# Kernel optimization log

Measured on AMD Instinct MI355X. Metric: run time of the kernel, lower is better.

The kernel has to match this reference:

```python
import jax, jax.numpy as jnp
import numpy as np

B, A, NC, DIR, LMAX, MAXZ, NORB = 8, 64, 128, 4, 2, 10, 14
NF = NC * DIR * (2 * LMAX + 1)   # 2560
O2 = NORB * NORB                 # 196
AO = A * NORB                    # 896
LOG2 = float(np.log(2.0))

def ssp(v):  # spk shifted softplus
    return jax.nn.softplus(v) - LOG2

def setup_inputs():
    key = jax.random.key(0)
    ks = jax.random.split(key, 12)
    Z = jax.random.randint(ks[0], (B, A), 1, MAXZ)
    idx = np.arange(A)
    nbh_np = np.stack([np.delete(idx, i) for i in range(A)], 0)  # [A, A-1]: all atoms except self
    nbh = jnp.asarray(np.broadcast_to(nbh_np[None], (B, A, A - 1)).copy(), dtype=jnp.int32)
    x = jax.random.normal(ks[1], (B, A, NC), jnp.float32)
    Vijkl = jax.random.normal(ks[2], (B, A, A - 1, NF), jnp.float32) * 0.1
    sc = 1.0 / np.sqrt(NF)
    W_off = jax.random.normal(ks[3], (NF, O2), jnp.float32) * sc
    b_off = jnp.zeros((O2,), jnp.float32)
    W_on = jax.random.normal(ks[4], (NF, O2), jnp.float32) * sc
    b_on = jnp.zeros((O2,), jnp.float32)
    W_ovoff = jax.random.normal(ks[5], (NF, O2), jnp.float32) * sc
    b_ovoff = jnp.zeros((O2,), jnp.float32)
    ov_emb = jax.random.normal(ks[6], (MAXZ, O2), jnp.float32) * 0.1  # trainable overlap onsite embedding
    orb_energies = jax.random.normal(ks[7], (MAXZ, NORB), jnp.float32)  # h0 energies
    s0_energies = jnp.ones((MAXZ, NORB), jnp.float32)                   # s0 init = ones
    W1 = jax.random.normal(ks[8], (NC, NC // 2), jnp.float32) / np.sqrt(NC)
    b1 = jnp.zeros((NC // 2,), jnp.float32)
    W2 = jax.random.normal(ks[9], (NC // 2, 1), jnp.float32) / np.sqrt(NC // 2)
    b2 = jnp.zeros((1,), jnp.float32)
    return {"Z": Z, "nbh": nbh, "x": x, "Vijkl": Vijkl,
            "W_off": W_off, "b_off": b_off, "W_on": W_on, "b_on": b_on,
            "W_ovoff": W_ovoff, "b_ovoff": b_ovoff, "ov_emb": ov_emb,
            "orb_energies": orb_energies, "s0_energies": s0_energies,
            "W1": W1, "b1": b1, "W2": W2, "b2": b2}

def reference(Z, nbh, x, Vijkl, W_off, b_off, W_on, b_on, W_ovoff, b_ovoff,
              ov_emb, orb_energies, s0_energies, W1, b1, W2, b2):
    # permutation that reorders neighbor slots (plus appended zero/self slot) into atom order
    ar = jnp.broadcast_to(jnp.arange(A, dtype=nbh.dtype)[None, :, None], (B, A, 1))
    sort_idx = jnp.argsort(jnp.concatenate([nbh, ar], axis=2), axis=2)  # [B,A,A]
    eyeA = jnp.eye(A, dtype=Vijkl.dtype)
    eyeAO = jnp.eye(AO, dtype=Vijkl.dtype)

    def assemble(off, on):
        # off: [B,A,A-1,O2] pair blocks; on: [B,A,O2] onsite blocks
        offz = jnp.concatenate([off, jnp.zeros((B, A, 1, O2), off.dtype)], axis=2)  # zero self block at slot A-1
        offg = jnp.take_along_axis(offz, sort_idx[..., None], axis=2)               # [B,A,A,O2]
        M = offg + eyeA[None, :, :, None] * on[:, :, None, :]
        M = M.reshape(B, A, A, NORB, NORB).transpose(0, 1, 3, 2, 4).reshape(B, AO, AO)
        return 0.5 * (M + M.transpose(0, 2, 1))

    # Hamiltonian: offsite Dense + onsite Dense mean-aggregated over pairs
    H_off = Vijkl @ W_off + b_off                       # [B,A,A-1,O2]
    H_on = jnp.mean(Vijkl @ W_on + b_on, axis=2)        # [B,A,O2]
    H = assemble(H_off, H_on)
    # h0 single-atom diagonal (orb mask is all-active -> full diagonal)
    H = H + eyeAO[None] * orb_energies[Z].reshape(B, 1, AO)

    # Overlap: offsite Dense + onsite embedding lookup
    S_off = Vijkl @ W_ovoff + b_ovoff
    S_on = ov_emb[Z]                                    # [B,A,O2]
    S = assemble(S_off, S_on)
    S = S + eyeAO[None] * s0_energies[Z].reshape(B, 1, AO)

    # energy head: Dense->ssp->Dense->ScaleShift(0,1), sum over atoms
    Ei = ssp(x @ W1 + b1) @ W2 + b2                     # [B,A,1]
    E = jnp.sum(Ei, axis=1)                             # [B,1]
    return H, S, E
```

## Files before the change

kernel.cpp:

```cpp
#include <hip/hip_runtime.h>

#define B_      8
#define A_      64
#define NPAIR   63
#define NC_     128
#define NF_     2560
#define O2_     196
#define NORB_   14
#define AO_     896
#define NCOLS   588
#define NSTORE  392
#define CSTRIDE 400
#define KSTEPS  80
#define NMACRO  20
#define BM      126
#define BN      640
#define MAC_BYTES 81920

typedef float f32x4 __attribute__((ext_vector_type(4)));
typedef int   v8i   __attribute__((ext_vector_type(8)));
typedef int   v4i   __attribute__((ext_vector_type(4)));

#define SCA 0x7F7F7F7F
#define SCB 0x7C7C7C7C

__device__ __forceinline__ unsigned f2bf(float f) {
    unsigned u = __builtin_bit_cast(unsigned, f);
    return (u + 0x7fffu + ((u >> 16) & 1u)) >> 16;
}

__global__ __launch_bounds__(512)
void prep_energy(const float* __restrict__ W_off, const float* __restrict__ W_ovoff,
                 const float* __restrict__ W_on, unsigned char* __restrict__ Bws,
                 const float* __restrict__ x, const float* __restrict__ W1,
                 const float* __restrict__ b1, const float* __restrict__ W2,
                 const float* __restrict__ b2, float* __restrict__ E) {
    const int t = threadIdx.x;
    if (blockIdx.x < KSTEPS) {
        __shared__ float wt[32 * BN];
        const int ks = blockIdx.x;
        for (int e = t; e < 32 * BN; e += 512) {
            int kl = e / BN, c = e - kl * BN;
            int kg = ks * 32 + kl;
            float v = 0.f;
            if (c < O2_)          v = W_off  [(size_t)kg * O2_ + c];
            else if (c < 2 * O2_) v = W_ovoff[(size_t)kg * O2_ + (c - O2_)];
            else if (c < 3 * O2_) v = W_on   [(size_t)kg * O2_ + (c - 2 * O2_)];
            wt[kl * BN + c] = v * 8.0f;
        }
        __syncthreads();
        unsigned char* out = Bws + (size_t)(ks >> 2) * MAC_BYTES + (ks & 3) * 32;
        for (int u = t; u < BN * 8; u += 512) {
            int n = u >> 3, q = u & 7;
            int w = __builtin_amdgcn_cvt_pk_fp8_f32(wt[(q*4+0)*BN+n], wt[(q*4+1)*BN+n], 0, false);
            w     = __builtin_amdgcn_cvt_pk_fp8_f32(wt[(q*4+2)*BN+n], wt[(q*4+3)*BN+n], w, true);
            *(int*)(out + (size_t)n * 128 + q * 4) = w;
        }
    } else {
        __shared__ float partial[8];
        const int b = blockIdx.x - KSTEPS;
        const int lane = t & 63;
        const int w = t >> 6;
        float esum = 0.f;
        for (int aa = 0; aa < 8; ++aa) {
            const int a = w * 8 + aa;
            const float* xr = x + (size_t)(b * A_ + a) * NC_;
            float hj = b1[lane];
            for (int k = 0; k < NC_; ++k) hj = fmaf(xr[k], W1[k * 64 + lane], hj);
            float sp = fmaxf(hj, 0.f) + log1pf(expf(-fabsf(hj))) - 0.69314718055994531f;
            float v = sp * W2[lane];
            for (int off = 32; off; off >>= 1) v += __shfl_down(v, off);
            if (lane == 0) esum += v + b2[0];
        }
        if (lane == 0) partial[w] = esum;
        __syncthreads();
        if (t == 0) {
            float e = 0.f;
            for (int k = 0; k < 8; ++k) e += partial[k];
            E[b] = e;
        }
    }
}

__global__ __launch_bounds__(512, 2)
void gemm_off(const float* __restrict__ V, const unsigned char* __restrict__ Bws,
              const float* __restrict__ b_off, const float* __restrict__ b_ovoff,
              const float* __restrict__ b_on, float* __restrict__ HSoff,
              float* __restrict__ Hon) {
    __shared__ alignas(16) float Af32[8][4096];
    __shared__ alignas(16) unsigned char Afp8[4 * 6144];
    __shared__ float HonLds[2][O2_];

    const int tid  = threadIdx.x;
    const int mt   = blockIdx.x;
    const int lane = tid & 63;
    const int wv   = tid >> 6;
    const int wm   = wv >> 2, wn = wv & 3;
    const int wvu  = __builtin_amdgcn_readfirstlane(wv);

    const int r0  = tid >> 3;
    const int r1c = (64 + r0) > 125 ? 125 : (64 + r0);
    const int sg  = tid & 7;
    const float* asrc0 = V + (size_t)(mt * BM + r0)  * NF_ + sg * 4;
    const float* asrc1 = V + (size_t)(mt * BM + r1c) * NF_ + sg * 4;

    const unsigned char* bbase = Bws + ((size_t)(wn * 160 + (lane & 15))) * 128 + (lane >> 4) * 32;
#define BLD(T_, nf_) (*(const v8i*)(bbase + (size_t)(T_) * MAC_BYTES + (nf_) * 2048))

    const unsigned aoff = (unsigned)(lane >> 4) * 6144 + (unsigned)(wm * 64 + (lane & 15)) * 48;

    f32x4 acc[4][10];
#pragma unroll
    for (int mf = 0; mf < 4; ++mf)
#pragma unroll
        for (int nf = 0; nf < 10; ++nf)
            acc[mf][nf] = (f32x4){0.f, 0.f, 0.f, 0.f};

    auto stage = [&](int slot, int k32) {
        __builtin_amdgcn_global_load_lds(
            (const __attribute__((address_space(1))) void*)(asrc0 + (size_t)k32 * 32),
            (__attribute__((address_space(3))) void*)(&Af32[slot][wvu * 256]), 16, 0, 0);
        __builtin_amdgcn_global_load_lds(
            (const __attribute__((address_space(1))) void*)(asrc1 + (size_t)k32 * 32),
            (__attribute__((address_space(3))) void*)(&Af32[slot][2048 + wvu * 256]), 16, 0, 0);
    };
    auto conv = [&](int slot, int sub) {
        const char* sp = (const char*)&Af32[slot][0];
        float4 f0 = *(const float4*)(sp + tid * 16);
        float4 f1 = *(const float4*)(sp + tid * 16 + 8192);
        int w0 = __builtin_amdgcn_cvt_pk_fp8_f32(f0.x, f0.y, 0, false);
        w0     = __builtin_amdgcn_cvt_pk_fp8_f32(f0.z, f0.w, w0, true);
        int w1 = __builtin_amdgcn_cvt_pk_fp8_f32(f1.x, f1.y, 0, false);
        w1     = __builtin_amdgcn_cvt_pk_fp8_f32(f1.z, f1.w, w1, true);
        *(int*)&Afp8[sub * 6144 + (tid >> 3) * 48 + (tid & 7) * 4] = w0;
        *(int*)&Afp8[sub * 6144 + (64 + (tid >> 3)) * 48 + (tid & 7) * 4] = w1;
    };

    union AV { v4i h[2]; v8i v; };
#define AFLD(dst_, mf_) { AV a_; \
    a_.h[0] = *(const v4i*)&Afp8[aoff + (mf_) * 768];      \
    a_.h[1] = *(const v4i*)&Afp8[aoff + (mf_) * 768 + 16]; \
    dst_ = a_.v; }

#define MFMA1(abf_, bq_, mf_, nf_) \
    acc[mf_][nf_] = __builtin_amdgcn_mfma_scale_f32_16x16x128_f8f6f4( \
        abf_, bq_, acc[mf_][nf_], 0, 0, 0, SCA, 0, SCB);

#define C4(bv_, nf_) { \
    __builtin_amdgcn_s_setprio(1); \
    MFMA1(af0, bv_, 0, nf_); MFMA1(af1, bv_, 1, nf_); \
    MFMA1(af2, bv_, 2, nf_); MFMA1(af3, bv_, 3, nf_); \
    __builtin_amdgcn_s_setprio(0); }

    v8i b0, b1, b2, b3, b4, af0, af1, af2, af3;

    stage(0, 0); stage(1, 1); stage(2, 2); stage(3, 3);
    b0 = BLD(0, 0); b1 = BLD(0, 1); b2 = BLD(0, 2); b3 = BLD(0, 3); b4 = BLD(0, 4);

    for (int T = 0; T < NMACRO; ++T) {
        const int sb = (T & 1) * 4;
        const int st = ((T + 1) & 1) * 4;
#pragma unroll
        for (int i = 0; i < 4; ++i) {
            asm volatile("s_waitcnt vmcnt(16)" ::: "memory");
            __builtin_amdgcn_sched_barrier(0);
            if (T < NMACRO - 1) stage(st + i, 4 * (T + 1) + i);
            else                stage(st + i, 76 + i);
            conv(sb + i, i);
        }
        asm volatile("s_waitcnt lgkmcnt(0)" ::: "memory");
        __builtin_amdgcn_sched_barrier(0);
        __builtin_amdgcn_s_barrier();
        __builtin_amdgcn_sched_barrier(0);

        AFLD(af0, 0); AFLD(af1, 1); AFLD(af2, 2); AFLD(af3, 3);
        C4(b0, 0); b0 = BLD(T, 5);
        C4(b1, 1); b1 = BLD(T, 6);
        C4(b2, 2); b2 = BLD(T, 7);
        C4(b3, 3); b3 = BLD(T, 8);
        C4(b4, 4); b4 = BLD(T, 9);
        C4(b0, 5); b0 = BLD(T + 1, 0);
        C4(b1, 6); b1 = BLD(T + 1, 1);
        C4(b2, 7); b2 = BLD(T + 1, 2);
        C4(b3, 8); b3 = BLD(T + 1, 3);
        C4(b4, 9); b4 = BLD(T + 1, 4);
        __builtin_amdgcn_sched_barrier(0);
        __builtin_amdgcn_s_barrier();
        __builtin_amdgcn_sched_barrier(0);
    }

    if (tid < 2 * O2_) HonLds[tid / O2_][tid % O2_] = 0.f;
    __syncthreads();

    const int c16 = lane & 15, rg = lane >> 4;
#pragma unroll
    for (int nf = 0; nf < 10; ++nf) {
        const int C = wn * 160 + nf * 16 + c16;
        if (C >= NSTORE) continue;
        const float bias = (C < O2_) ? b_off[C] : b_ovoff[C - O2_];
#pragma unroll
        for (int mf = 0; mf < 4; ++mf) {
            const int L = wm * 64 + mf * 16 + rg * 4;
#pragma unroll
            for (int jj = 0; jj < 4; ++jj) {
                const int row = L + jj;
                if (row < BM)
                    HSoff[(size_t)(mt * BM + row) * CSTRIDE + C] = acc[mf][nf][jj] + bias;
            }
        }
    }
#pragma unroll
    for (int nf = 0; nf < 10; ++nf) {
        const int C = wn * 160 + nf * 16 + c16;
        if (C < NSTORE || C >= NCOLS) continue;
        const int cc = C - NSTORE;
        float s0 = 0.f, s1 = 0.f;
#pragma unroll
        for (int mf = 0; mf < 4; ++mf) {
            const int L = wm * 64 + mf * 16 + rg * 4;
#pragma unroll
            for (int jj = 0; jj < 4; ++jj) {
                const int row = L + jj;
                const float v = acc[mf][nf][jj];
                if (row < NPAIR)       s0 += v;
                else if (row < BM)     s1 += v;
            }
        }
        s0 += __shfl_down(s0, 32); s0 += __shfl_down(s0, 16);
        s1 += __shfl_down(s1, 32); s1 += __shfl_down(s1, 16);
        if (lane < 16) {
            atomicAdd(&HonLds[0][cc], s0);
            atomicAdd(&HonLds[1][cc], s1);
        }
    }
    __syncthreads();
    if (tid < 2 * O2_) {
        const int atom = tid / O2_, c = tid % O2_;
        Hon[(size_t)(mt * 2 + atom) * O2_ + c] =
            HonLds[atom][c] * (1.f / (float)NPAIR) + b_on[c];
    }
#undef BLD
#undef AFLD
#undef MFMA1
#undef C4
}

__global__ __launch_bounds__(256)
void assemble_k(const float* __restrict__ HSoff, const float* __restrict__ Hon,
                const int* __restrict__ Z, const float* __restrict__ ov_emb,
                const float* __restrict__ orbE, const float* __restrict__ s0E,
                float* __restrict__ H, float* __restrict__ S) {
    __shared__ float Ai[NPAIR * 197];
    __shared__ float Bj[2][16 * 200];
    __shared__ float Dg[O2_];
    __shared__ float Dd[NORB_];

    const int bid = blockIdx.x;
    const int h = bid & 1, i = (bid >> 1) & 63, b = bid >> 7;
    const int t = threadIdx.x;
    const int g = b * A_ + i;
    const int z = Z[g];
    float* out = (h ? S : H) + (size_t)b * AO_ * AO_;

    const float* abase = HSoff + (size_t)g * NPAIR * CSTRIDE + h * O2_;
    for (int u = t; u < NPAIR * O2_; u += 256) {
        int jj = u / O2_, e = u - jj * O2_;
        Ai[jj * 197 + e] = abase[(size_t)jj * CSTRIDE + e];
    }
    if (t < O2_)   Dg[t] = h ? ov_emb[(size_t)z * O2_ + t]   : Hon[(size_t)g * O2_ + t];
    if (t < NORB_) Dd[t] = h ? s0E[(size_t)z * NORB_ + t]    : orbE[(size_t)z * NORB_ + t];

    auto stageB = [&](int buf, int jc) {
        for (int u = t; u < 16 * O2_; u += 256) {
            int jl = u / O2_, e = u - jl * O2_;
            int j = jc * 16 + jl;
            if (j != i) {
                int idx = (i < j) ? i : i - 1;
                Bj[buf][jl * 200 + e] =
                    HSoff[((size_t)(b * A_ + j) * NPAIR + idx) * CSTRIDE + h * O2_ + e];
            }
        }
    };
    stageB(0, 0);
    __syncthreads();

    const int tj = t / NORB_, tq = t - tj * NORB_;
    for (int jc = 0; jc < 4; ++jc) {
        if (jc < 3) stageB((jc + 1) & 1, jc + 1);
        if (t < 224) {
            const int j = jc * 16 + tj;
            const int cur = jc & 1;
#pragma unroll
            for (int p = 0; p < NORB_; ++p) {
                float v;
                if (j == i) {
                    v = 0.5f * (Dg[p * NORB_ + tq] + Dg[tq * NORB_ + p]);
                    if (p == tq) v += Dd[p];
                } else {
                    int jj = (j < i) ? j : j - 1;
                    v = 0.5f * (Ai[jj * 197 + p * NORB_ + tq] + Bj[cur][tj * 200 + tq * NORB_ + p]);
                }
                out[(size_t)(i * NORB_ + p) * AO_ + jc * 224 + t] = v;
            }
        }
        __syncthreads();
    }
}

extern "C" void kernel_launch(void* const* d_in, const int* in_sizes, int n_in,
                              void* d_out, int out_size, void* d_ws, size_t ws_size,
                              hipStream_t stream) {
    const int*   Z       = (const int*)  d_in[0];
    const float* x       = (const float*)d_in[2];
    const float* V       = (const float*)d_in[3];
    const float* W_off   = (const float*)d_in[4];
    const float* b_off   = (const float*)d_in[5];
    const float* W_on    = (const float*)d_in[6];
    const float* b_on    = (const float*)d_in[7];
    const float* W_ovoff = (const float*)d_in[8];
    const float* b_ovoff = (const float*)d_in[9];
    const float* ov_emb  = (const float*)d_in[10];
    const float* orbE    = (const float*)d_in[11];
    const float* s0E     = (const float*)d_in[12];
    const float* W1      = (const float*)d_in[13];
    const float* b1      = (const float*)d_in[14];
    const float* W2      = (const float*)d_in[15];
    const float* b2      = (const float*)d_in[16];

    float* H = (float*)d_out;
    float* S = H + (size_t)B_ * AO_ * AO_;
    float* E = S + (size_t)B_ * AO_ * AO_;

    char* ws = (char*)d_ws;
    unsigned char* Bws = (unsigned char*)ws;
    float* HSoff = (float*)(ws + (size_t)4  * 1024 * 1024);
    float* Hon   = (float*)(ws + (size_t)60 * 1024 * 1024);

    prep_energy<<<KSTEPS + B_, 512, 0, stream>>>(W_off, W_ovoff, W_on, Bws,
                                                 x, W1, b1, W2, b2, E);
    gemm_off   <<<256,  512, 0, stream>>>(V, Bws, b_off, b_ovoff, b_on, HSoff, Hon);
    assemble_k <<<1024, 256, 0, stream>>>(HSoff, Hon, Z, ov_emb, orbE, s0E, H, S);
}
```

Before: 288.2 us.

## Pre-convert V to swizzled fp8 tiles in prep kernel, simplify GEMM pipeline

Moves the fp32-to-fp8 conversion of the activation matrix out of the GEMM main loop into a separate bandwidth-bound pass in the prep kernel. That pass writes fp8 tiles with an XOR-swizzled layout, and the GEMM loads them directly into LDS with double buffering and no per-step conversion. This removes the LDS round trip and conversion work from the MFMA loop. In exchange it adds an extra write and read of an ~80MB fp8 intermediate in global memory.

```diff
diff --git a/kernel.cpp b/kernel.cpp
--- a/kernel.cpp
+++ b/kernel.cpp
@@ -16,10 +16,10 @@
 #define BM      126
 #define BN      640
 #define MAC_BYTES 81920
+#define ATILE   16384
 
 typedef float f32x4 __attribute__((ext_vector_type(4)));
 typedef int   v8i   __attribute__((ext_vector_type(8)));
-typedef int   v4i   __attribute__((ext_vector_type(4)));
 
 #define SCA 0x7F7F7F7F
 #define SCB 0x7C7C7C7C
@@ -30,11 +30,12 @@
 }
 
 __global__ __launch_bounds__(512)
-void prep_energy(const float* __restrict__ W_off, const float* __restrict__ W_ovoff,
-                 const float* __restrict__ W_on, unsigned char* __restrict__ Bws,
-                 const float* __restrict__ x, const float* __restrict__ W1,
-                 const float* __restrict__ b1, const float* __restrict__ W2,
-                 const float* __restrict__ b2, float* __restrict__ E) {
+void prep_all(const float* __restrict__ W_off, const float* __restrict__ W_ovoff,
+              const float* __restrict__ W_on, unsigned char* __restrict__ Bws,
+              const float* __restrict__ x, const float* __restrict__ W1,
+              const float* __restrict__ b1, const float* __restrict__ W2,
+              const float* __restrict__ b2, float* __restrict__ E,
+              const float* __restrict__ V, unsigned char* __restrict__ Aws) {
     const int t = threadIdx.x;
     if (blockIdx.x < KSTEPS) {
         __shared__ float wt[32 * BN];
@@ -56,7 +57,7 @@
             w     = __builtin_amdgcn_cvt_pk_fp8_f32(wt[(q*4+2)*BN+n], wt[(q*4+3)*BN+n], w, true);
             *(int*)(out + (size_t)n * 128 + q * 4) = w;
         }
-    } else {
+    } else if (blockIdx.x < KSTEPS + B_) {
         __shared__ float partial[8];
         const int b = blockIdx.x - KSTEPS;
         const int lane = t & 63;
@@ -79,16 +80,35 @@
             for (int k = 0; k < 8; ++k) e += partial[k];
             E[b] = e;
         }
+    } else {
+        const int u = (blockIdx.x - KSTEPS - B_) * 512 + t;
+        const int R = u / 160, c16 = u - R * 160;
+        const float* src = V + (size_t)R * NF_ + c16 * 16;
+        float4 f0 = ((const float4*)src)[0];
+        float4 f1 = ((const float4*)src)[1];
+        float4 f2 = ((const float4*)src)[2];
+        float4 f3 = ((const float4*)src)[3];
+        int4 w;
+        w.x = __builtin_amdgcn_cvt_pk_fp8_f32(f0.x, f0.y, 0, false);
+        w.x = __builtin_amdgcn_cvt_pk_fp8_f32(f0.z, f0.w, w.x, true);
+        w.y = __builtin_amdgcn_cvt_pk_fp8_f32(f1.x, f1.y, 0, false);
+        w.y = __builtin_amdgcn_cvt_pk_fp8_f32(f1.z, f1.w, w.y, true);
+        w.z = __builtin_amdgcn_cvt_pk_fp8_f32(f2.x, f2.y, 0, false);
+        w.z = __builtin_amdgcn_cvt_pk_fp8_f32(f2.z, f2.w, w.z, true);
+        w.w = __builtin_amdgcn_cvt_pk_fp8_f32(f3.x, f3.y, 0, false);
+        w.w = __builtin_amdgcn_cvt_pk_fp8_f32(f3.z, f3.w, w.w, true);
+        const int mtile = R / BM, row = R - mtile * BM;
+        const int T = c16 >> 3, s = c16 & 7;
+        *(int4*)(Aws + ((size_t)(mtile * NMACRO + T) << 14) + row * 128 + s * 16) = w;
     }
 }
 
 __global__ __launch_bounds__(512, 2)
-void gemm_off(const float* __restrict__ V, const unsigned char* __restrict__ Bws,
+void gemm_off(const unsigned char* __restrict__ Aws, const unsigned char* __restrict__ Bws,
               const float* __restrict__ b_off, const float* __restrict__ b_ovoff,
               const float* __restrict__ b_on, float* __restrict__ HSoff,
               float* __restrict__ Hon) {
-    __shared__ alignas(16) float Af32[8][4096];
-    __shared__ alignas(16) unsigned char Afp8[4 * 6144];
+    __shared__ alignas(16) unsigned char Afp8[2][ATILE];
     __shared__ float HonLds[2][O2_];
 
     const int tid  = threadIdx.x;
@@ -98,16 +118,18 @@
     const int wm   = wv >> 2, wn = wv & 3;
     const int wvu  = __builtin_amdgcn_readfirstlane(wv);
 
-    const int r0  = tid >> 3;
-    const int r1c = (64 + r0) > 125 ? 125 : (64 + r0);
-    const int sg  = tid & 7;
-    const float* asrc0 = V + (size_t)(mt * BM + r0)  * NF_ + sg * 4;
-    const float* asrc1 = V + (size_t)(mt * BM + r1c) * NF_ + sg * 4;
+    const int row0 = tid >> 3, seg = tid & 7;
+    const int row1 = 64 + row0, rowc1 = row1 > 125 ? 125 : row1;
+    const unsigned off0 = (unsigned)(row0 * 128 + (((seg >> 1) ^ (row0 & 3)) << 5) + (seg & 1) * 16);
+    const unsigned off1 = (unsigned)(rowc1 * 128 + (((seg >> 1) ^ (rowc1 & 3)) << 5) + (seg & 1) * 16);
+    const unsigned char* atile0 = Aws + (size_t)mt * NMACRO * ATILE;
 
     const unsigned char* bbase = Bws + ((size_t)(wn * 160 + (lane & 15))) * 128 + (lane >> 4) * 32;
 #define BLD(T_, nf_) (*(const v8i*)(bbase + (size_t)(T_) * MAC_BYTES + (nf_) * 2048))
 
-    const unsigned aoff = (unsigned)(lane >> 4) * 6144 + (unsigned)(wm * 64 + (lane & 15)) * 48;
+    const unsigned abase = (unsigned)(wm * 64 * 128 + (lane & 15) * 128 +
+                                      (((lane >> 4) ^ (lane & 3)) << 5));
+#define AFLD(dst_, buf_, mf_) dst_ = *(const v8i*)&Afp8[buf_][abase + (mf_) * 2048];
 
     f32x4 acc[4][10];
 #pragma unroll
@@ -116,31 +138,15 @@
         for (int nf = 0; nf < 10; ++nf)
             acc[mf][nf] = (f32x4){0.f, 0.f, 0.f, 0.f};
 
-    auto stage = [&](int slot, int k32) {
+    auto stage = [&](int buf, int T) {
+        const unsigned char* tp = atile0 + (size_t)T * ATILE;
         __builtin_amdgcn_global_load_lds(
-            (const __attribute__((address_space(1))) void*)(asrc0 + (size_t)k32 * 32),
-            (__attribute__((address_space(3))) void*)(&Af32[slot][wvu * 256]), 16, 0, 0);
+            (const __attribute__((address_space(1))) void*)(tp + off0),
+            (__attribute__((address_space(3))) void*)(&Afp8[buf][wvu * 1024]), 16, 0, 0);
         __builtin_amdgcn_global_load_lds(
-            (const __attribute__((address_space(1))) void*)(asrc1 + (size_t)k32 * 32),
-            (__attribute__((address_space(3))) void*)(&Af32[slot][2048 + wvu * 256]), 16, 0, 0);
+            (const __attribute__((address_space(1))) void*)(tp + off1),
+            (__attribute__((address_space(3))) void*)(&Afp8[buf][8192 + wvu * 1024]), 16, 0, 0);
     };
-    auto conv = [&](int slot, int sub) {
-        const char* sp = (const char*)&Af32[slot][0];
-        float4 f0 = *(const float4*)(sp + tid * 16);
-        float4 f1 = *(const float4*)(sp + tid * 16 + 8192);
-        int w0 = __builtin_amdgcn_cvt_pk_fp8_f32(f0.x, f0.y, 0, false);
-        w0     = __builtin_amdgcn_cvt_pk_fp8_f32(f0.z, f0.w, w0, true);
-        int w1 = __builtin_amdgcn_cvt_pk_fp8_f32(f1.x, f1.y, 0, false);
-        w1     = __builtin_amdgcn_cvt_pk_fp8_f32(f1.z, f1.w, w1, true);
-        *(int*)&Afp8[sub * 6144 + (tid >> 3) * 48 + (tid & 7) * 4] = w0;
-        *(int*)&Afp8[sub * 6144 + (64 + (tid >> 3)) * 48 + (tid & 7) * 4] = w1;
-    };
-
-    union AV { v4i h[2]; v8i v; };
-#define AFLD(dst_, mf_) { AV a_; \
-    a_.h[0] = *(const v4i*)&Afp8[aoff + (mf_) * 768];      \
-    a_.h[1] = *(const v4i*)&Afp8[aoff + (mf_) * 768 + 16]; \
-    dst_ = a_.v; }
 
 #define MFMA1(abf_, bq_, mf_, nf_) \
     acc[mf_][nf_] = __builtin_amdgcn_mfma_scale_f32_16x16x128_f8f6f4( \
@@ -154,26 +160,21 @@
 
     v8i b0, b1, b2, b3, b4, af0, af1, af2, af3;
 
-    stage(0, 0); stage(1, 1); stage(2, 2); stage(3, 3);
+    stage(0, 0);
     b0 = BLD(0, 0); b1 = BLD(0, 1); b2 = BLD(0, 2); b3 = BLD(0, 3); b4 = BLD(0, 4);
-
+    asm volatile("s_waitcnt vmcnt(5)" ::: "memory");
+    __builtin_amdgcn_sched_barrier(0);
+    __builtin_amdgcn_s_barrier();
+    __builtin_amdgcn_sched_barrier(0);
+
+    int cur = 0;
     for (int T = 0; T < NMACRO; ++T) {
-        const int sb = (T & 1) * 4;
-        const int st = ((T + 1) & 1) * 4;
-#pragma unroll
-        for (int i = 0; i < 4; ++i) {
-            asm volatile("s_waitcnt vmcnt(16)" ::: "memory");
-            __builtin_amdgcn_sched_barrier(0);
-            if (T < NMACRO - 1) stage(st + i, 4 * (T + 1) + i);
-            else                stage(st + i, 76 + i);
-            conv(sb + i, i);
-        }
+        AFLD(af0, cur, 0); AFLD(af1, cur, 1); AFLD(af2, cur, 2); AFLD(af3, cur, 3);
         asm volatile("s_waitcnt lgkmcnt(0)" ::: "memory");
         __builtin_amdgcn_sched_barrier(0);
-        __builtin_amdgcn_s_barrier();
-        __builtin_amdgcn_sched_barrier(0);
-
-        AFLD(af0, 0); AFLD(af1, 1); AFLD(af2, 2); AFLD(af3, 3);
+
+        stage(cur ^ 1, T + 1 < NMACRO ? T + 1 : NMACRO - 1);
+
         C4(b0, 0); b0 = BLD(T, 5);
         C4(b1, 1); b1 = BLD(T, 6);
         C4(b2, 2); b2 = BLD(T, 7);
@@ -184,9 +185,12 @@
         C4(b2, 7); b2 = BLD(T + 1, 2);
         C4(b3, 8); b3 = BLD(T + 1, 3);
         C4(b4, 9); b4 = BLD(T + 1, 4);
+
+        asm volatile("s_waitcnt vmcnt(10)" ::: "memory");
         __builtin_amdgcn_sched_barrier(0);
         __builtin_amdgcn_s_barrier();
         __builtin_amdgcn_sched_barrier(0);
+        cur ^= 1;
     }
 
     if (tid < 2 * O2_) HonLds[tid / O2_][tid % O2_] = 0.f;
@@ -333,11 +337,13 @@
 
     char* ws = (char*)d_ws;
     unsigned char* Bws = (unsigned char*)ws;
-    float* HSoff = (float*)(ws + (size_t)4  * 1024 * 1024);
-    float* Hon   = (float*)(ws + (size_t)60 * 1024 * 1024);
-
-    prep_energy<<<KSTEPS + B_, 512, 0, stream>>>(W_off, W_ovoff, W_on, Bws,
-                                                 x, W1, b1, W2, b2, E);
-    gemm_off   <<<256,  512, 0, stream>>>(V, Bws, b_off, b_ovoff, b_on, HSoff, Hon);
-    assemble_k <<<1024, 256, 0, stream>>>(HSoff, Hon, Z, ov_emb, orbE, s0E, H, S);
-}
+    unsigned char* Aws = (unsigned char*)(ws + (size_t)4 * 1024 * 1024);
+    float* HSoff = (float*)(ws + (size_t)88  * 1024 * 1024);
+    float* Hon   = (float*)(ws + (size_t)142 * 1024 * 1024);
+
+    const int conv_blocks = (32256 * 160) / 512;
+    prep_all  <<<KSTEPS + B_ + conv_blocks, 512, 0, stream>>>(
+        W_off, W_ovoff, W_on, Bws, x, W1, b1, W2, b2, E, V, Aws);
+    gemm_off  <<<256,  512, 0, stream>>>(Aws, Bws, b_off, b_ovoff, b_on, HSoff, Hon);
+    assemble_k<<<1024, 256, 0, stream>>>(HSoff, Hon, Z, ov_emb, orbE, s0E, H, S);
+}
```

New measurement: 271.3 us. 5.8% less time.

## Restructure A-tile staging into fp32 ring plus swizzled double-buffered fp8 tile

Applied to the files above, without the earlier changes.

Replaces the 8-slot fp32 staging buffer and interleaved per-substep convert loop with a 4-slot fp32 ring and a double-buffered fp8 A tile. All four k-substeps of the next macro step are loaded at once, and the fp8 conversion runs after this step's MFMAs. The fp8 layout now uses 128-byte rows with an XOR swizzle, so each fragment is one 32-byte LDS read instead of two 16-byte reads, and each macro step needs one barrier instead of two. The cost is a shorter global-load lookahead: the next step's loads are issued and waited on within the same iteration, so latency is hidden only by one macro step of MFMAs.

```diff
diff --git a/kernel.cpp b/kernel.cpp
--- a/kernel.cpp
+++ b/kernel.cpp
@@ -19,15 +19,9 @@
 
 typedef float f32x4 __attribute__((ext_vector_type(4)));
 typedef int   v8i   __attribute__((ext_vector_type(8)));
-typedef int   v4i   __attribute__((ext_vector_type(4)));
 
 #define SCA 0x7F7F7F7F
 #define SCB 0x7C7C7C7C
-
-__device__ __forceinline__ unsigned f2bf(float f) {
-    unsigned u = __builtin_bit_cast(unsigned, f);
-    return (u + 0x7fffu + ((u >> 16) & 1u)) >> 16;
-}
 
 __global__ __launch_bounds__(512)
 void prep_energy(const float* __restrict__ W_off, const float* __restrict__ W_ovoff,
@@ -87,8 +81,8 @@
               const float* __restrict__ b_off, const float* __restrict__ b_ovoff,
               const float* __restrict__ b_on, float* __restrict__ HSoff,
               float* __restrict__ Hon) {
-    __shared__ alignas(16) float Af32[8][4096];
-    __shared__ alignas(16) unsigned char Afp8[4 * 6144];
+    __shared__ alignas(16) float Ring[4 * 4096];
+    __shared__ alignas(16) unsigned char Afp8[2][16384];
     __shared__ float HonLds[2][O2_];
 
     const int tid  = threadIdx.x;
@@ -98,16 +92,17 @@
     const int wm   = wv >> 2, wn = wv & 3;
     const int wvu  = __builtin_amdgcn_readfirstlane(wv);
 
-    const int r0  = tid >> 3;
-    const int r1c = (64 + r0) > 125 ? 125 : (64 + r0);
-    const int sg  = tid & 7;
-    const float* asrc0 = V + (size_t)(mt * BM + r0)  * NF_ + sg * 4;
-    const float* asrc1 = V + (size_t)(mt * BM + r1c) * NF_ + sg * 4;
+    const int srow0 = tid >> 3;
+    const int srow1 = 64 + srow0 > 125 ? 125 : 64 + srow0;
+    const float* src0 = V + (size_t)(mt * BM + srow0) * NF_ + (tid & 7) * 4;
+    const float* src1 = V + (size_t)(mt * BM + srow1) * NF_ + (tid & 7) * 4;
 
     const unsigned char* bbase = Bws + ((size_t)(wn * 160 + (lane & 15))) * 128 + (lane >> 4) * 32;
 #define BLD(T_, nf_) (*(const v8i*)(bbase + (size_t)(T_) * MAC_BYTES + (nf_) * 2048))
 
-    const unsigned aoff = (unsigned)(lane >> 4) * 6144 + (unsigned)(wm * 64 + (lane & 15)) * 48;
+    const unsigned abase = (unsigned)(wm * 8192 + (lane & 15) * 128 +
+                                      (((lane >> 4) ^ (lane & 3)) << 5));
+#define AFLD(dst_, buf_, mf_) dst_ = *(const v8i*)&Afp8[buf_][abase + (mf_) * 2048];
 
     f32x4 acc[4][10];
 #pragma unroll
@@ -116,31 +111,33 @@
         for (int nf = 0; nf < 10; ++nf)
             acc[mf][nf] = (f32x4){0.f, 0.f, 0.f, 0.f};
 
-    auto stage = [&](int slot, int k32) {
-        __builtin_amdgcn_global_load_lds(
-            (const __attribute__((address_space(1))) void*)(asrc0 + (size_t)k32 * 32),
-            (__attribute__((address_space(3))) void*)(&Af32[slot][wvu * 256]), 16, 0, 0);
-        __builtin_amdgcn_global_load_lds(
-            (const __attribute__((address_space(1))) void*)(asrc1 + (size_t)k32 * 32),
-            (__attribute__((address_space(3))) void*)(&Af32[slot][2048 + wvu * 256]), 16, 0, 0);
+    auto stage = [&](int T1) {
+#pragma unroll
+        for (int s = 0; s < 4; ++s) {
+            const int k32 = T1 * 4 + s;
+            __builtin_amdgcn_global_load_lds(
+                (const __attribute__((address_space(1))) void*)(src0 + (size_t)k32 * 32),
+                (__attribute__((address_space(3))) void*)(&Ring[s * 4096 + wvu * 256]), 16, 0, 0);
+            __builtin_amdgcn_global_load_lds(
+                (const __attribute__((address_space(1))) void*)(src1 + (size_t)k32 * 32),
+                (__attribute__((address_space(3))) void*)(&Ring[s * 4096 + 2048 + wvu * 256]), 16, 0, 0);
+        }
     };
-    auto conv = [&](int slot, int sub) {
-        const char* sp = (const char*)&Af32[slot][0];
-        float4 f0 = *(const float4*)(sp + tid * 16);
-        float4 f1 = *(const float4*)(sp + tid * 16 + 8192);
-        int w0 = __builtin_amdgcn_cvt_pk_fp8_f32(f0.x, f0.y, 0, false);
-        w0     = __builtin_amdgcn_cvt_pk_fp8_f32(f0.z, f0.w, w0, true);
-        int w1 = __builtin_amdgcn_cvt_pk_fp8_f32(f1.x, f1.y, 0, false);
-        w1     = __builtin_amdgcn_cvt_pk_fp8_f32(f1.z, f1.w, w1, true);
-        *(int*)&Afp8[sub * 6144 + (tid >> 3) * 48 + (tid & 7) * 4] = w0;
-        *(int*)&Afp8[sub * 6144 + (64 + (tid >> 3)) * 48 + (tid & 7) * 4] = w1;
+    auto conv = [&](int dstbuf) {
+#pragma unroll
+        for (int r = 0; r < 2; ++r) {
+            const int row = r * 64 + (tid >> 3);
+            const unsigned wrbase = (unsigned)(row * 128) ;
+            const unsigned rsw = (unsigned)(row & 3);
+#pragma unroll
+            for (int s = 0; s < 4; ++s) {
+                float4 f = *(const float4*)&Ring[s * 4096 + r * 2048 + tid * 4];
+                int w = __builtin_amdgcn_cvt_pk_fp8_f32(f.x, f.y, 0, false);
+                w     = __builtin_amdgcn_cvt_pk_fp8_f32(f.z, f.w, w, true);
+                *(int*)&Afp8[dstbuf][wrbase + (((unsigned)s ^ rsw) << 5) + (tid & 7) * 4] = w;
+            }
+        }
     };
-
-    union AV { v4i h[2]; v8i v; };
-#define AFLD(dst_, mf_) { AV a_; \
-    a_.h[0] = *(const v4i*)&Afp8[aoff + (mf_) * 768];      \
-    a_.h[1] = *(const v4i*)&Afp8[aoff + (mf_) * 768 + 16]; \
-    dst_ = a_.v; }
 
 #define MFMA1(abf_, bq_, mf_, nf_) \
     acc[mf_][nf_] = __builtin_amdgcn_mfma_scale_f32_16x16x128_f8f6f4( \
@@ -154,26 +151,21 @@
 
     v8i b0, b1, b2, b3, b4, af0, af1, af2, af3;
 
-    stage(0, 0); stage(1, 1); stage(2, 2); stage(3, 3);
+    stage(0);
     b0 = BLD(0, 0); b1 = BLD(0, 1); b2 = BLD(0, 2); b3 = BLD(0, 3); b4 = BLD(0, 4);
-
+    asm volatile("s_waitcnt vmcnt(5)" ::: "memory");
+    __builtin_amdgcn_sched_barrier(0);
+    conv(0);
+    asm volatile("s_waitcnt lgkmcnt(0)" ::: "memory");
+    __builtin_amdgcn_s_barrier();
+    __builtin_amdgcn_sched_barrier(0);
+
+    int cur = 0;
     for (int T = 0; T < NMACRO; ++T) {
-        const int sb = (T & 1) * 4;
-        const int st = ((T + 1) & 1) * 4;
-#pragma unroll
-        for (int i = 0; i < 4; ++i) {
-            asm volatile("s_waitcnt vmcnt(16)" ::: "memory");
-            __builtin_amdgcn_sched_barrier(0);
-            if (T < NMACRO - 1) stage(st + i, 4 * (T + 1) + i);
-            else                stage(st + i, 76 + i);
-            conv(sb + i, i);
-        }
-        asm volatile("s_waitcnt lgkmcnt(0)" ::: "memory");
-        __builtin_amdgcn_sched_barrier(0);
-        __builtin_amdgcn_s_barrier();
-        __builtin_amdgcn_sched_barrier(0);
-
-        AFLD(af0, 0); AFLD(af1, 1); AFLD(af2, 2); AFLD(af3, 3);
+        AFLD(af0, cur, 0); AFLD(af1, cur, 1); AFLD(af2, cur, 2); AFLD(af3, cur, 3);
+
+        if (T < NMACRO - 1) stage(T + 1);
+
         C4(b0, 0); b0 = BLD(T, 5);
         C4(b1, 1); b1 = BLD(T, 6);
         C4(b2, 2); b2 = BLD(T, 7);
@@ -184,9 +176,17 @@
         C4(b2, 7); b2 = BLD(T + 1, 2);
         C4(b3, 8); b3 = BLD(T + 1, 3);
         C4(b4, 9); b4 = BLD(T + 1, 4);
+
+        if (T < NMACRO - 1) {
+            asm volatile("s_waitcnt vmcnt(10)" ::: "memory");
+            __builtin_amdgcn_sched_barrier(0);
+            conv(cur ^ 1);
+        }
+        asm volatile("s_waitcnt lgkmcnt(0)" ::: "memory");
         __builtin_amdgcn_sched_barrier(0);
         __builtin_amdgcn_s_barrier();
         __builtin_amdgcn_sched_barrier(0);
+        cur ^= 1;
     }
 
     if (tid < 2 * O2_) HonLds[tid / O2_][tid % O2_] = 0.f;
```

Result: faster. 267.5 us (-7.2%).
